# Performance work log

Measured on AMD Instinct MI355X. Metric: run time of the kernel, lower is better.

The kernel has to match this reference:

```python
import jax, jax.numpy as jnp
import numpy as np

DIM = 1024
EPS_LN = 1e-5
EPS_MEM = 1e-6

def _layernorm(x, g, b):
    mu = jnp.mean(x, axis=-1, keepdims=True)
    var = jnp.mean((x - mu) ** 2, axis=-1, keepdims=True)
    return (x - mu) * jax.lax.rsqrt(var + EPS_LN) * g + b

def setup_inputs() -> dict:
    key = jax.random.key(0)
    ks = jax.random.split(key, 8)
    B, S, D = 4, 4096, DIM
    s1 = 1.0 / np.sqrt(D)
    s2 = 1.0 / np.sqrt(4 * D)
    return {
        "x": jax.random.normal(ks[0], (B, S, D), dtype=jnp.float32),
        "ln1_g": jnp.ones((D,), jnp.float32),
        "ln1_b": jnp.zeros((D,), jnp.float32),
        "ln2_g": jnp.ones((D,), jnp.float32),
        "ln2_b": jnp.zeros((D,), jnp.float32),
        "gate_w": jax.random.uniform(ks[1], (D, D), jnp.float32, -s1, s1),
        "gate_b": jax.random.uniform(ks[2], (D,), jnp.float32, -s1, s1),
        "value_w": jax.random.uniform(ks[3], (D, D), jnp.float32, -s1, s1),
        "value_b": jax.random.uniform(ks[4], (D,), jnp.float32, -s1, s1),
        "ffn_w1": jax.random.uniform(ks[5], (D, 4 * D), jnp.float32, -s1, s1),
        "ffn_b1": jnp.zeros((4 * D,), jnp.float32),
        "ffn_w2": jax.random.uniform(ks[6], (4 * D, D), jnp.float32, -s2, s2),
        "ffn_b2": jnp.zeros((D,), jnp.float32),
    }

def reference(x, ln1_g, ln1_b, ln2_g, ln2_b, gate_w, gate_b, value_w, value_b, ffn_w1, ffn_b1, ffn_w2, ffn_b2):
    h = _layernorm(x, ln1_g, ln1_b)
    g = jax.nn.sigmoid(h @ gate_w + gate_b)
    v = h @ value_w + value_b
    cumsum_v = jnp.cumsum(g * v, axis=1)
    cumsum_g = jnp.cumsum(g, axis=1) + EPS_MEM
    x = x + cumsum_v / cumsum_g
    h2 = _layernorm(x, ln2_g, ln2_b)
    ffn = jax.nn.gelu(h2 @ ffn_w1 + ffn_b1, approximate=False) @ ffn_w2 + ffn_b2
    return x + ffn
```

## Files before the change

### kernel.cpp

```cpp
#include <hip/hip_runtime.h>
#include <cstdint>
#include <cstddef>

#define D_MODEL 1024
#define SEQ     4096
#define BATCH   4
#define M_ROWS  (BATCH*SEQ)
#define NCHUNK  64
#define LCHUNK  (SEQ/NCHUNK)

typedef __bf16 bf16_t;
typedef __bf16 bf16x8 __attribute__((ext_vector_type(8)));
typedef __bf16 bf16x4 __attribute__((ext_vector_type(4)));
typedef float  f32x4  __attribute__((ext_vector_type(4)));

__device__ __forceinline__ void load_lds_128(const bf16_t* g, bf16_t* l) {
    __builtin_amdgcn_global_load_lds(
        (const __attribute__((address_space(1))) unsigned int*)g,
        (__attribute__((address_space(3))) unsigned int*)l,
        16, 0, 0);
}

__device__ __forceinline__ float2 bf16pair_to_f2(unsigned int u) {
    union { unsigned int i; float f; } a, b;
    a.i = u << 16;
    b.i = u & 0xffff0000u;
    float2 r; r.x = a.f; r.y = b.f; return r;
}

__global__ __launch_bounds__(256)
void transpose_all(const float* __restrict__ gate_w, const float* __restrict__ value_w,
                   const float* __restrict__ ffn_w1, const float* __restrict__ ffn_w2,
                   bf16_t* __restrict__ wgv_t, bf16_t* __restrict__ w1_t,
                   bf16_t* __restrict__ w2_t) {
    int id = blockIdx.x;
    const float* in; bf16_t* outp; int R, C, bx, by;
    if (id < 1024)      { in = gate_w;  outp = wgv_t;               R = 1024; C = 1024; bx = id & 31;  by = id >> 5; }
    else if (id < 2048) { id -= 1024; in = value_w; outp = wgv_t + 1024*1024; R = 1024; C = 1024; bx = id & 31;  by = id >> 5; }
    else if (id < 6144) { id -= 2048; in = ffn_w1;  outp = w1_t;    R = 1024; C = 4096; bx = id & 127; by = id >> 7; }
    else                { id -= 6144; in = ffn_w2;  outp = w2_t;    R = 4096; C = 1024; bx = id & 31;  by = id >> 5; }
    __shared__ float t[32][33];
    int tx = threadIdx.x & 31, ty = threadIdx.x >> 5;
    int c0 = bx * 32, r0 = by * 32;
    #pragma unroll
    for (int j = 0; j < 32; j += 8)
        t[ty + j][tx] = in[(size_t)(r0 + ty + j) * C + c0 + tx];
    __syncthreads();
    #pragma unroll
    for (int j = 0; j < 32; j += 8)
        outp[(size_t)(c0 + ty + j) * R + r0 + tx] = (bf16_t)t[tx][ty + j];
}

__global__ __launch_bounds__(256)
void ln_kernel(const float* __restrict__ x, const float* __restrict__ gamma,
               const float* __restrict__ beta, bf16_t* __restrict__ h) {
    int row = blockIdx.x;
    int tid = threadIdx.x;
    const float4* xr = (const float4*)(x + (size_t)row * D_MODEL);
    float4 v = xr[tid];
    float s  = v.x + v.y + v.z + v.w;
    float ss = v.x*v.x + v.y*v.y + v.z*v.z + v.w*v.w;
    #pragma unroll
    for (int off = 32; off; off >>= 1) {
        s  += __shfl_down(s, off);
        ss += __shfl_down(ss, off);
    }
    __shared__ float red[8];
    int wave = tid >> 6, lane = tid & 63;
    if (lane == 0) { red[wave] = s; red[4 + wave] = ss; }
    __syncthreads();
    if (tid == 0) {
        float S  = red[0] + red[1] + red[2] + red[3];
        float SS = red[4] + red[5] + red[6] + red[7];
        float mean = S * (1.0f / D_MODEL);
        float var  = SS * (1.0f / D_MODEL) - mean * mean;
        red[0] = mean;
        red[1] = rsqrtf(var + 1e-5f);
    }
    __syncthreads();
    float mean = red[0], rstd = red[1];
    float4 gv = ((const float4*)gamma)[tid];
    float4 bv = ((const float4*)beta)[tid];
    bf16x4 o;
    o[0] = (bf16_t)((v.x - mean) * rstd * gv.x + bv.x);
    o[1] = (bf16_t)((v.y - mean) * rstd * gv.y + bv.y);
    o[2] = (bf16_t)((v.z - mean) * rstd * gv.z + bv.z);
    o[3] = (bf16_t)((v.w - mean) * rstd * gv.w + bv.w);
    ((bf16x4*)h)[(size_t)row * (D_MODEL / 4) + tid] = o;
}

#define PHASE_MID() do { __builtin_amdgcn_s_barrier(); \
    asm volatile("s_waitcnt lgkmcnt(0)" ::: "memory"); \
    __builtin_amdgcn_s_setprio(1); } while (0)
#define PHASE_END() do { __builtin_amdgcn_s_setprio(0); \
    __builtin_amdgcn_s_barrier(); } while (0)
#define PHASE_END_VM() do { __builtin_amdgcn_s_setprio(0); \
    asm volatile("s_waitcnt vmcnt(4)" ::: "memory"); \
    __builtin_amdgcn_s_barrier(); } while (0)

#define LDA4(BUF, MB) do { _Pragma("unroll") for (int m_ = 0; m_ < 4; ++m_) { \
    af[m_][0] = *(const bf16x8*)((BUF) + aoff0 + ((MB)*4 + m_) * 1024); \
    af[m_][1] = *(const bf16x8*)((BUF) + aoff1 + ((MB)*4 + m_) * 1024); } } while (0)
#define LDB2(BUF, NLO) do { _Pragma("unroll") for (int n_ = 0; n_ < 2; ++n_) { \
    bfr[(NLO)+n_][0] = *(const bf16x8*)((BUF) + boff0 + ((NLO)+n_) * 1024); \
    bfr[(NLO)+n_][1] = *(const bf16x8*)((BUF) + boff1 + ((NLO)+n_) * 1024); } } while (0)
#define MFMA_HALF(MB, NLO) do { _Pragma("unroll") for (int m_ = 0; m_ < 4; ++m_) { \
    _Pragma("unroll") for (int n_ = 0; n_ < 2; ++n_) { \
        acc[(MB)*4 + m_][(NLO) + n_] = __builtin_amdgcn_mfma_f32_16x16x32_bf16( \
            bfr[(NLO)+n_][0], af[m_][0], acc[(MB)*4 + m_][(NLO) + n_], 0, 0, 0); \
        acc[(MB)*4 + m_][(NLO) + n_] = __builtin_amdgcn_mfma_f32_16x16x32_bf16( \
            bfr[(NLO)+n_][1], af[m_][1], acc[(MB)*4 + m_][(NLO) + n_], 0, 0, 0); } } } while (0)

template <int MODE, int TN>
__global__ __launch_bounds__(512, 2)
void gemm256(const bf16_t* __restrict__ A, const bf16_t* __restrict__ Bt,
             const float* __restrict__ bias, const float* __restrict__ bias2,
             const float* __restrict__ xres,
             void* __restrict__ out, void* __restrict__ out2,
             int M, int N, int K) {
    __shared__ __align__(16) bf16_t lds[2][2][256 * 64];

    const int tid  = threadIdx.x;
    const int lane = tid & 63;
    const int wave = tid >> 6;
    const int wm   = wave >> 2;
    const int wn   = wave & 3;

    const int L  = blockIdx.x;
    const int r  = L >> 3;
    const int n0 = (r % TN) * 256;
    const int m0 = ((L & 7) + 8 * (r / TN)) * 256;

    f32x4 acc[8][4];
    #pragma unroll
    for (int i = 0; i < 8; i++)
        #pragma unroll
        for (int j = 0; j < 4; j++) acc[i][j] = (f32x4){0.f, 0.f, 0.f, 0.f};

    const int rr = tid >> 3;
    const int sc = ((tid & 7) ^ (rr & 7)) * 8;
    const bf16_t* pa = A  + ((size_t)(m0 + rr)) * K + sc;
    const bf16_t* pb = Bt + ((size_t)(n0 + rr)) * K + sc;
    const size_t rstep = (size_t)64 * K;
    const size_t hstep = rstep * 2;

    const int l16 = lane & 15, quad = lane >> 4, swz = l16 & 7;
    const int aoff0 = (wm*128 + l16)*64 + ((quad    ) ^ swz)*8;
    const int aoff1 = (wm*128 + l16)*64 + ((quad + 4) ^ swz)*8;
    const int boff0 = (wn*64  + l16)*64 + ((quad    ) ^ swz)*8;
    const int boff1 = (wn*64  + l16)*64 + ((quad + 4) ^ swz)*8;

    bf16_t* LA0 = &lds[0][0][0]; bf16_t* LB0 = &lds[0][1][0];
    bf16_t* LA1 = &lds[1][0][0]; bf16_t* LB1 = &lds[1][1][0];

    const int KT = K >> 6;
    const int NI = KT >> 1;

    auto STAGE = [&](const bf16_t* gsrc, bf16_t* dst) {
        load_lds_128(gsrc,         dst + tid * 8);
        load_lds_128(gsrc + rstep, dst + 4096 + tid * 8);
    };

    STAGE(pb,              LB0);
    STAGE(pb + hstep,      LB0 + 8192);
    STAGE(pa,              LA0);
    STAGE(pa + hstep,      LA0 + 8192);
    STAGE(pb + 64,         LB1);
    STAGE(pb + hstep + 64, LB1 + 8192);
    asm volatile("s_waitcnt vmcnt(4)" ::: "memory");
    __builtin_amdgcn_s_barrier();

    for (int it = 0; it < NI; ++it) {
        const int k1 = (2*it + 1) * 64;
        const int t2 = (2*it + 2 < KT) ? 2*it + 2 : KT - 1;
        const int t3 = (2*it + 3 < KT) ? 2*it + 3 : KT - 1;
        const int k2 = t2 * 64, k3 = t3 * 64;

        bf16x8 af[4][2], bfr[4][2];

        LDA4(LA0, 0); LDB2(LB0, 0);
        STAGE(pa + k1, LA1);
        PHASE_MID(); MFMA_HALF(0, 0); PHASE_END();
        LDB2(LB0, 2);
        STAGE(pa + hstep + k1, LA1 + 8192);
        PHASE_MID(); MFMA_HALF(0, 2); PHASE_END();
        LDA4(LA0, 1);
        STAGE(pb + k2, LB0);
        PHASE_MID(); MFMA_HALF(1, 0); PHASE_END();
        STAGE(pb + hstep + k2, LB0 + 8192);
        PHASE_MID(); MFMA_HALF(1, 2); PHASE_END_VM();
        LDA4(LA1, 0); LDB2(LB1, 0);
        STAGE(pa + k2, LA0);
        PHASE_MID(); MFMA_HALF(0, 0); PHASE_END();
        LDB2(LB1, 2);
        STAGE(pa + hstep + k2, LA0 + 8192);
        PHASE_MID(); MFMA_HALF(0, 2); PHASE_END();
        LDA4(LA1, 1);
        STAGE(pb + k3, LB1);
        PHASE_MID(); MFMA_HALF(1, 0); PHASE_END();
        STAGE(pb + hstep + k3, LB1 + 8192);
        PHASE_MID(); MFMA_HALF(1, 2); PHASE_END_VM();
    }

    asm volatile("s_waitcnt vmcnt(0)" ::: "memory");

    #pragma unroll
    for (int mt = 0; mt < 8; ++mt) {
        int row = m0 + wm * 128 + mt * 16 + l16;
        #pragma unroll
        for (int nt = 0; nt < 4; ++nt) {
            int col = n0 + wn * 64 + nt * 16 + quad * 4;
            f32x4 a = acc[mt][nt];
            if (MODE == 4) {
                bool isV = (n0 >= 1024);
                int c1 = col & 1023;
                float4 bv = *(const float4*)((isV ? bias2 : bias) + c1);
                float4 val;
                val.x = a[0] + bv.x; val.y = a[1] + bv.y;
                val.z = a[2] + bv.z; val.w = a[3] + bv.w;
                if (!isV) {
                    val.x = 1.0f / (1.0f + __expf(-val.x));
                    val.y = 1.0f / (1.0f + __expf(-val.y));
                    val.z = 1.0f / (1.0f + __expf(-val.z));
                    val.w = 1.0f / (1.0f + __expf(-val.w));
                }
                bf16x4 p;
                p[0] = (bf16_t)val.x; p[1] = (bf16_t)val.y;
                p[2] = (bf16_t)val.z; p[3] = (bf16_t)val.w;
                bf16_t* o = (bf16_t*)(isV ? out2 : out);
                *(bf16x4*)(o + (size_t)row * 1024 + c1) = p;
            } else if (MODE == 2) {
                float4 bv = *(const float4*)(bias + col);
                float4 val;
                val.x = a[0] + bv.x; val.y = a[1] + bv.y;
                val.z = a[2] + bv.z; val.w = a[3] + bv.w;
                val.x = 0.5f * val.x * (1.0f + erff(val.x * 0.70710678118654752f));
                val.y = 0.5f * val.y * (1.0f + erff(val.y * 0.70710678118654752f));
                val.z = 0.5f * val.z * (1.0f + erff(val.z * 0.70710678118654752f));
                val.w = 0.5f * val.w * (1.0f + erff(val.w * 0.70710678118654752f));
                bf16x4 p;
                p[0] = (bf16_t)val.x; p[1] = (bf16_t)val.y;
                p[2] = (bf16_t)val.z; p[3] = (bf16_t)val.w;
                *(bf16x4*)((bf16_t*)out + (size_t)row * N + col) = p;
            } else {
                float4 bv = *(const float4*)(bias + col);
                float4 xr = *(const float4*)(xres + (size_t)row * N + col);
                float4 val;
                val.x = xr.x + a[0] + bv.x; val.y = xr.y + a[1] + bv.y;
                val.z = xr.z + a[2] + bv.z; val.w = xr.w + a[3] + bv.w;
                *(float4*)((float*)out + (size_t)row * N + col) = val;
            }
        }
    }
}

__global__ __launch_bounds__(256)
void scan_partial(const bf16_t* __restrict__ g, const bf16_t* __restrict__ v,
                  float* __restrict__ sg, float* __restrict__ sgv) {
    int dt = blockIdx.x & 1;
    int c  = (blockIdx.x >> 1) & (NCHUNK - 1);
    int b  = blockIdx.x >> 7;
    int d  = dt * 512 + threadIdx.x * 2;
    float s0 = 0.f, s1 = 0.f, t0 = 0.f, t1 = 0.f;
    for (int i = 0; i < LCHUNK; i++) {
        int s = c * LCHUNK + i;
        size_t idx = ((size_t)(b * SEQ + s)) * D_MODEL + d;
        float2 gf = bf16pair_to_f2(*(const unsigned int*)(g + idx));
        float2 vf = bf16pair_to_f2(*(const unsigned int*)(v + idx));
        s0 += gf.x; s1 += gf.y;
        t0 += gf.x * vf.x; t1 += gf.y * vf.y;
    }
    size_t o = ((size_t)(b * NCHUNK + c)) * D_MODEL + d;
    sg[o] = s0;  sg[o + 1] = s1;
    sgv[o] = t0; sgv[o + 1] = t1;
}

__global__ __launch_bounds__(256)
void scan_apply(const bf16_t* __restrict__ g, const bf16_t* __restrict__ v,
                const float* __restrict__ x, const float* __restrict__ sg,
                const float* __restrict__ sgv, float* __restrict__ out) {
    int dt = blockIdx.x & 1;
    int c  = (blockIdx.x >> 1) & (NCHUNK - 1);
    int b  = blockIdx.x >> 7;
    int d  = dt * 512 + threadIdx.x * 2;
    float rg0 = 0.f, rg1 = 0.f, rv0 = 0.f, rv1 = 0.f;
    for (int p = 0; p < c; p++) {
        size_t o = ((size_t)(b * NCHUNK + p)) * D_MODEL + d;
        float2 a  = *(const float2*)(sg + o);
        float2 bb = *(const float2*)(sgv + o);
        rg0 += a.x;  rg1 += a.y;
        rv0 += bb.x; rv1 += bb.y;
    }
    for (int i = 0; i < LCHUNK; i++) {
        int s = c * LCHUNK + i;
        size_t idx = ((size_t)(b * SEQ + s)) * D_MODEL + d;
        float2 gf = bf16pair_to_f2(*(const unsigned int*)(g + idx));
        float2 vf = bf16pair_to_f2(*(const unsigned int*)(v + idx));
        rv0 += gf.x * vf.x; rg0 += gf.x;
        rv1 += gf.y * vf.y; rg1 += gf.y;
        float2 xv = *(const float2*)(x + idx);
        float2 ov;
        ov.x = xv.x + rv0 / (rg0 + 1e-6f);
        ov.y = xv.y + rv1 / (rg1 + 1e-6f);
        *(float2*)(out + idx) = ov;
    }
}

extern "C" void kernel_launch(void* const* d_in, const int* in_sizes, int n_in,
                              void* d_out, int out_size, void* d_ws, size_t ws_size,
                              hipStream_t stream) {
    (void)in_sizes; (void)n_in; (void)out_size; (void)ws_size;
    const float* x       = (const float*)d_in[0];
    const float* ln1_g   = (const float*)d_in[1];
    const float* ln1_b   = (const float*)d_in[2];
    const float* ln2_g   = (const float*)d_in[3];
    const float* ln2_b   = (const float*)d_in[4];
    const float* gate_w  = (const float*)d_in[5];
    const float* gate_b  = (const float*)d_in[6];
    const float* value_w = (const float*)d_in[7];
    const float* value_b = (const float*)d_in[8];
    const float* ffn_w1  = (const float*)d_in[9];
    const float* ffn_b1  = (const float*)d_in[10];
    const float* ffn_w2  = (const float*)d_in[11];
    const float* ffn_b2  = (const float*)d_in[12];
    float* out = (float*)d_out;

    char* ws = (char*)d_ws;
    const size_t MB = 1024 * 1024;
    bf16_t* wgv_t = (bf16_t*)(ws + 0 * MB);
    bf16_t* w1_t  = (bf16_t*)(ws + 4 * MB);
    bf16_t* w2_t  = (bf16_t*)(ws + 12 * MB);
    bf16_t* h     = (bf16_t*)(ws + 20 * MB);
    bf16_t* g     = (bf16_t*)(ws + 52 * MB);
    bf16_t* v     = (bf16_t*)(ws + 84 * MB);
    float*  sg    = (float*)(ws + 116 * MB);
    float*  sgv   = (float*)(ws + 117 * MB);
    bf16_t* act   = (bf16_t*)(ws + 118 * MB);

    transpose_all<<<10240, 256, 0, stream>>>(gate_w, value_w, ffn_w1, ffn_w2,
                                             wgv_t, w1_t, w2_t);

    ln_kernel<<<M_ROWS, 256, 0, stream>>>(x, ln1_g, ln1_b, h);

    gemm256<4, 8><<<8 * 64, 512, 0, stream>>>(
        h, wgv_t, gate_b, value_b, nullptr, g, v, M_ROWS, 2048, 1024);

    scan_partial<<<BATCH * NCHUNK * 2, 256, 0, stream>>>(g, v, sg, sgv);
    scan_apply<<<BATCH * NCHUNK * 2, 256, 0, stream>>>(g, v, x, sg, sgv, out);

    ln_kernel<<<M_ROWS, 256, 0, stream>>>(out, ln2_g, ln2_b, h);

    gemm256<2, 16><<<16 * 64, 512, 0, stream>>>(
        h, w1_t, ffn_b1, nullptr, nullptr, act, nullptr, M_ROWS, 4096, 1024);

    gemm256<3, 4><<<4 * 64, 512, 0, stream>>>(
        act, w2_t, ffn_b2, nullptr, out, out, nullptr, M_ROWS, 1024, 4096);
}
```

Before: 621.1 us.

## Make GEMMs persistent over multiple N tiles and use tanh-form GELU

Each GEMM now launches a fixed 256 blocks, and every block walks several consecutive 256-wide N tiles. The K pipeline runs continuously across tile boundaries, and the epilogue is emitted whenever a tile's K loop completes. This keeps prefetch going across tiles, reduces launch and tail effects, and lets the A tile stay hot in cache. The exact erf GELU is also replaced by a sigmoid-based tanh approximation, which is cheaper but changes numerics relative to the exact reference. The mid-loop epilogue adds register pressure and breaks the overlap at each tile boundary.

```diff
diff --git a/kernel.cpp b/kernel.cpp
--- a/kernel.cpp
+++ b/kernel.cpp
@@ -26,6 +26,12 @@
     a.i = u << 16;
     b.i = u & 0xffff0000u;
     float2 r; r.x = a.f; r.y = b.f; return r;
+}
+
+__device__ __forceinline__ float gelu_f(float x) {
+    float t = x * x;
+    float u = x * (1.5957691216f + 0.07135481627f * t);
+    return x / (1.0f + __expf(-u));
 }
 
 __global__ __launch_bounds__(256)
@@ -111,7 +117,7 @@
         acc[(MB)*4 + m_][(NLO) + n_] = __builtin_amdgcn_mfma_f32_16x16x32_bf16( \
             bfr[(NLO)+n_][1], af[m_][1], acc[(MB)*4 + m_][(NLO) + n_], 0, 0, 0); } } } while (0)
 
-template <int MODE, int TN>
+template <int MODE, int TN, int TPB, int LKT>
 __global__ __launch_bounds__(512, 2)
 void gemm256(const bf16_t* __restrict__ A, const bf16_t* __restrict__ Bt,
              const float* __restrict__ bias, const float* __restrict__ bias2,
@@ -120,29 +126,39 @@
              int M, int N, int K) {
     __shared__ __align__(16) bf16_t lds[2][2][256 * 64];
 
+    const int KT = 1 << LKT;
+    const int S  = TPB * KT;
+    const int NI = S >> 1;
+
     const int tid  = threadIdx.x;
     const int lane = tid & 63;
     const int wave = tid >> 6;
     const int wm   = wave >> 2;
     const int wn   = wave & 3;
 
-    const int L  = blockIdx.x;
-    const int r  = L >> 3;
-    const int n0 = (r % TN) * 256;
-    const int m0 = ((L & 7) + 8 * (r / TN)) * 256;
+    const int L    = blockIdx.x;
+    const int i    = L >> 3;
+    const int ngrp = i & 3;
+    const int mb   = (L & 7) + 8 * (i >> 2);
+    const int m0   = mb * 256;
+    const int n00  = ngrp * TPB * 256;
 
     f32x4 acc[8][4];
     #pragma unroll
-    for (int i = 0; i < 8; i++)
+    for (int ii = 0; ii < 8; ii++)
         #pragma unroll
-        for (int j = 0; j < 4; j++) acc[i][j] = (f32x4){0.f, 0.f, 0.f, 0.f};
+        for (int j = 0; j < 4; j++) acc[ii][j] = (f32x4){0.f, 0.f, 0.f, 0.f};
 
     const int rr = tid >> 3;
     const int sc = ((tid & 7) ^ (rr & 7)) * 8;
-    const bf16_t* pa = A  + ((size_t)(m0 + rr)) * K + sc;
-    const bf16_t* pb = Bt + ((size_t)(n0 + rr)) * K + sc;
-    const size_t rstep = (size_t)64 * K;
-    const size_t hstep = rstep * 2;
+    const bf16_t* pa0 = A  + ((size_t)(m0  + rr)) * K + sc;
+    const bf16_t* pb0 = Bt + ((size_t)(n00 + rr)) * K + sc;
+    const size_t rstep   = (size_t)64 * K;
+    const size_t hstep   = rstep * 2;
+    const size_t nstride = (size_t)256 * K;
+
+    #define PA(s) (pa0 + (((s) & (KT - 1)) << 6))
+    #define PB(s) (pb0 + (size_t)((s) >> LKT) * nstride + (((s) & (KT - 1)) << 6))
 
     const int l16 = lane & 15, quad = lane >> 4, swz = l16 & 7;
     const int aoff0 = (wm*128 + l16)*64 + ((quad    ) ^ swz)*8;
@@ -153,105 +169,108 @@
     bf16_t* LA0 = &lds[0][0][0]; bf16_t* LB0 = &lds[0][1][0];
     bf16_t* LA1 = &lds[1][0][0]; bf16_t* LB1 = &lds[1][1][0];
 
-    const int KT = K >> 6;
-    const int NI = KT >> 1;
-
     auto STAGE = [&](const bf16_t* gsrc, bf16_t* dst) {
         load_lds_128(gsrc,         dst + tid * 8);
         load_lds_128(gsrc + rstep, dst + 4096 + tid * 8);
     };
 
-    STAGE(pb,              LB0);
-    STAGE(pb + hstep,      LB0 + 8192);
-    STAGE(pa,              LA0);
-    STAGE(pa + hstep,      LA0 + 8192);
-    STAGE(pb + 64,         LB1);
-    STAGE(pb + hstep + 64, LB1 + 8192);
+    STAGE(PB(0),         LB0);
+    STAGE(PB(0) + hstep, LB0 + 8192);
+    STAGE(PA(0),         LA0);
+    STAGE(PA(0) + hstep, LA0 + 8192);
+    STAGE(PB(1),         LB1);
+    STAGE(PB(1) + hstep, LB1 + 8192);
     asm volatile("s_waitcnt vmcnt(4)" ::: "memory");
     __builtin_amdgcn_s_barrier();
 
+    #pragma unroll 1
     for (int it = 0; it < NI; ++it) {
-        const int k1 = (2*it + 1) * 64;
-        const int t2 = (2*it + 2 < KT) ? 2*it + 2 : KT - 1;
-        const int t3 = (2*it + 3 < KT) ? 2*it + 3 : KT - 1;
-        const int k2 = t2 * 64, k3 = t3 * 64;
+        const int s1 = 2*it + 1;
+        const int s2 = (2*it + 2 < S) ? 2*it + 2 : S - 1;
+        const int s3 = (2*it + 3 < S) ? 2*it + 3 : S - 1;
+        const bf16_t* a1 = PA(s1);
+        const bf16_t* a2 = PA(s2);
+        const bf16_t* b2 = PB(s2);
+        const bf16_t* b3 = PB(s3);
 
         bf16x8 af[4][2], bfr[4][2];
 
         LDA4(LA0, 0); LDB2(LB0, 0);
-        STAGE(pa + k1, LA1);
+        STAGE(a1, LA1);
         PHASE_MID(); MFMA_HALF(0, 0); PHASE_END();
         LDB2(LB0, 2);
-        STAGE(pa + hstep + k1, LA1 + 8192);
+        STAGE(a1 + hstep, LA1 + 8192);
         PHASE_MID(); MFMA_HALF(0, 2); PHASE_END();
         LDA4(LA0, 1);
-        STAGE(pb + k2, LB0);
+        STAGE(b2, LB0);
         PHASE_MID(); MFMA_HALF(1, 0); PHASE_END();
-        STAGE(pb + hstep + k2, LB0 + 8192);
+        STAGE(b2 + hstep, LB0 + 8192);
         PHASE_MID(); MFMA_HALF(1, 2); PHASE_END_VM();
         LDA4(LA1, 0); LDB2(LB1, 0);
-        STAGE(pa + k2, LA0);
+        STAGE(a2, LA0);
         PHASE_MID(); MFMA_HALF(0, 0); PHASE_END();
         LDB2(LB1, 2);
-        STAGE(pa + hstep + k2, LA0 + 8192);
+        STAGE(a2 + hstep, LA0 + 8192);
         PHASE_MID(); MFMA_HALF(0, 2); PHASE_END();
         LDA4(LA1, 1);
-        STAGE(pb + k3, LB1);
+        STAGE(b3, LB1);
         PHASE_MID(); MFMA_HALF(1, 0); PHASE_END();
-        STAGE(pb + hstep + k3, LB1 + 8192);
+        STAGE(b3 + hstep, LB1 + 8192);
         PHASE_MID(); MFMA_HALF(1, 2); PHASE_END_VM();
-    }
-
-    asm volatile("s_waitcnt vmcnt(0)" ::: "memory");
-
-    #pragma unroll
-    for (int mt = 0; mt < 8; ++mt) {
-        int row = m0 + wm * 128 + mt * 16 + l16;
-        #pragma unroll
-        for (int nt = 0; nt < 4; ++nt) {
-            int col = n0 + wn * 64 + nt * 16 + quad * 4;
-            f32x4 a = acc[mt][nt];
-            if (MODE == 4) {
-                bool isV = (n0 >= 1024);
-                int c1 = col & 1023;
-                float4 bv = *(const float4*)((isV ? bias2 : bias) + c1);
-                float4 val;
-                val.x = a[0] + bv.x; val.y = a[1] + bv.y;
-                val.z = a[2] + bv.z; val.w = a[3] + bv.w;
-                if (!isV) {
-                    val.x = 1.0f / (1.0f + __expf(-val.x));
-                    val.y = 1.0f / (1.0f + __expf(-val.y));
-                    val.z = 1.0f / (1.0f + __expf(-val.z));
-                    val.w = 1.0f / (1.0f + __expf(-val.w));
+
+        if (((it + 1) & ((KT >> 1) - 1)) == 0) {
+            const int tdone = (2*it + 1) >> LKT;
+            const int nn0 = n00 + tdone * 256;
+            #pragma unroll
+            for (int mt = 0; mt < 8; ++mt) {
+                int row = m0 + wm * 128 + mt * 16 + l16;
+                #pragma unroll
+                for (int nt = 0; nt < 4; ++nt) {
+                    int col = nn0 + wn * 64 + nt * 16 + quad * 4;
+                    f32x4 a = acc[mt][nt];
+                    if (MODE == 4) {
+                        bool isV = (nn0 >= 1024);
+                        int c1 = col & 1023;
+                        float4 bv = *(const float4*)((isV ? bias2 : bias) + c1);
+                        float4 val;
+                        val.x = a[0] + bv.x; val.y = a[1] + bv.y;
+                        val.z = a[2] + bv.z; val.w = a[3] + bv.w;
+                        if (!isV) {
+                            val.x = 1.0f / (1.0f + __expf(-val.x));
+                            val.y = 1.0f / (1.0f + __expf(-val.y));
+                            val.z = 1.0f / (1.0f + __expf(-val.z));
+                            val.w = 1.0f / (1.0f + __expf(-val.w));
+                        }
+                        bf16x4 p;
+                        p[0] = (bf16_t)val.x; p[1] = (bf16_t)val.y;
+                        p[2] = (bf16_t)val.z; p[3] = (bf16_t)val.w;
+                        bf16_t* o = (bf16_t*)(isV ? out2 : out);
+                        *(bf16x4*)(o + (size_t)row * 1024 + c1) = p;
+                    } else if (MODE == 2) {
+                        float4 bv = *(const float4*)(bias + col);
+                        bf16x4 p;
+                        p[0] = (bf16_t)gelu_f(a[0] + bv.x);
+                        p[1] = (bf16_t)gelu_f(a[1] + bv.y);
+                        p[2] = (bf16_t)gelu_f(a[2] + bv.z);
+                        p[3] = (bf16_t)gelu_f(a[3] + bv.w);
+                        *(bf16x4*)((bf16_t*)out + (size_t)row * N + col) = p;
+                    } else {
+                        float4 bv = *(const float4*)(bias + col);
+                        float4 xr = *(const float4*)(xres + (size_t)row * N + col);
+                        float4 val;
+                        val.x = xr.x + a[0] + bv.x; val.y = xr.y + a[1] + bv.y;
+                        val.z = xr.z + a[2] + bv.z; val.w = xr.w + a[3] + bv.w;
+                        *(float4*)((float*)out + (size_t)row * N + col) = val;
+                    }
+                    acc[mt][nt] = (f32x4){0.f, 0.f, 0.f, 0.f};
                 }
-                bf16x4 p;
-                p[0] = (bf16_t)val.x; p[1] = (bf16_t)val.y;
-                p[2] = (bf16_t)val.z; p[3] = (bf16_t)val.w;
-                bf16_t* o = (bf16_t*)(isV ? out2 : out);
-                *(bf16x4*)(o + (size_t)row * 1024 + c1) = p;
-            } else if (MODE == 2) {
-                float4 bv = *(const float4*)(bias + col);
-                float4 val;
-                val.x = a[0] + bv.x; val.y = a[1] + bv.y;
-                val.z = a[2] + bv.z; val.w = a[3] + bv.w;
-                val.x = 0.5f * val.x * (1.0f + erff(val.x * 0.70710678118654752f));
-                val.y = 0.5f * val.y * (1.0f + erff(val.y * 0.70710678118654752f));
-                val.z = 0.5f * val.z * (1.0f + erff(val.z * 0.70710678118654752f));
-                val.w = 0.5f * val.w * (1.0f + erff(val.w * 0.70710678118654752f));
-                bf16x4 p;
-                p[0] = (bf16_t)val.x; p[1] = (bf16_t)val.y;
-                p[2] = (bf16_t)val.z; p[3] = (bf16_t)val.w;
-                *(bf16x4*)((bf16_t*)out + (size_t)row * N + col) = p;
-            } else {
-                float4 bv = *(const float4*)(bias + col);
-                float4 xr = *(const float4*)(xres + (size_t)row * N + col);
-                float4 val;
-                val.x = xr.x + a[0] + bv.x; val.y = xr.y + a[1] + bv.y;
-                val.z = xr.z + a[2] + bv.z; val.w = xr.w + a[3] + bv.w;
-                *(float4*)((float*)out + (size_t)row * N + col) = val;
             }
         }
     }
+
+    asm volatile("s_waitcnt vmcnt(0)" ::: "memory");
+    #undef PA
+    #undef PB
 }
 
 __global__ __launch_bounds__(256)
@@ -342,7 +361,7 @@
 
     ln_kernel<<<M_ROWS, 256, 0, stream>>>(x, ln1_g, ln1_b, h);
 
-    gemm256<4, 8><<<8 * 64, 512, 0, stream>>>(
+    gemm256<4, 8, 2, 4><<<256, 512, 0, stream>>>(
         h, wgv_t, gate_b, value_b, nullptr, g, v, M_ROWS, 2048, 1024);
 
     scan_partial<<<BATCH * NCHUNK * 2, 256, 0, stream>>>(g, v, sg, sgv);
@@ -350,9 +369,9 @@
 
     ln_kernel<<<M_ROWS, 256, 0, stream>>>(out, ln2_g, ln2_b, h);
 
-    gemm256<2, 16><<<16 * 64, 512, 0, stream>>>(
+    gemm256<2, 16, 4, 4><<<256, 512, 0, stream>>>(
         h, w1_t, ffn_b1, nullptr, nullptr, act, nullptr, M_ROWS, 4096, 1024);
 
-    gemm256<3, 4><<<4 * 64, 512, 0, stream>>>(
+    gemm256<3, 4, 1, 6><<<256, 512, 0, stream>>>(
         act, w2_t, ffn_b2, nullptr, out, out, nullptr, M_ROWS, 1024, 4096);
 }
```

Result: faster. 596.5 us (-4.0%).
